# Kernel optimization log

Hardware: AMD Instinct MI355X
Metric: run time of the kernel (lower is better)

The kernel has to match this reference:

```python
import jax, jax.numpy as jnp
import numpy as np

D = 256    # lstm_encoder_size
B = 1024   # batch (number of agents/trajectories)
T = 512    # prediction horizon (recurrence steps)
EPS = 1e-5


def setup_inputs() -> dict:
    key = jax.random.key(0)
    k = jax.random.split(key, 10)
    s = 1.0 / np.sqrt(D)
    return {
        "KS_ALL": jax.random.normal(k[0], (1, B, D), jnp.float32),
        "next_vf": jax.random.normal(k[1], (B, T), jnp.float32),
        # Koopman operators (torch Linear stores [out, in]; no bias)
        "A_w": jax.random.normal(k[2], (D, D), jnp.float32) * (0.4 * s),  # contractive
        "B_w": jax.random.normal(k[3], (D, 1), jnp.float32) * s,
        # decoder params (liner_dec=False)
        "W0": jax.random.normal(k[4], (2 * D, D), jnp.float32) * s,
        "b0": jnp.zeros((2 * D,), jnp.float32),
        "W1": jax.random.normal(k[5], (D, 2 * D), jnp.float32) / np.sqrt(2.0 * D),
        "b1": jnp.zeros((D,), jnp.float32),
        "ln_g": jnp.ones((D,), jnp.float32),
        "ln_b": jnp.zeros((D,), jnp.float32),
        "W2": jax.random.normal(k[6], (D, D), jnp.float32) * s,
        "b2": jnp.zeros((D,), jnp.float32),
        "W3": jax.random.normal(k[7], (3, D), jnp.float32) * s,
        "b3": jnp.zeros((3,), jnp.float32),
    }


def _layer_norm(x, g, b):
    mu = jnp.mean(x, axis=-1, keepdims=True)
    var = jnp.var(x, axis=-1, keepdims=True)
    return (x - mu) * jax.lax.rsqrt(var + EPS) * g + b


def reference(KS_ALL, next_vf, A_w, B_w, W0, b0, W1, b1, ln_g, ln_b, W2, b2, W3, b3):
    # train_flag=True -> use only the first time slice of KS_ALL
    ks0 = KS_ALL[0]                 # [B, D]
    u = next_vf.T                   # [T, B] time-major, matches permute(1,0,2)
    b_vec = B_w[:, 0]               # [D]  (Linear(1, D) on scalar input)

    def step(ks, u_t):
        ks_new = ks @ A_w.T + u_t[:, None] * b_vec[None, :]  # [B, D]
        return ks_new, ks_new

    _, ks_seq = jax.lax.scan(step, ks0, u)                   # [T, B, D]
    KS_pre = jnp.concatenate([ks0[None], ks_seq], axis=0)    # [T+1, B, D]

    # nonlinear decoder (eval mode: dropout is identity; use_elu=True)
    s1 = jnp.tanh(KS_pre @ W0.T + b0)          # [T+1, B, 2D]
    s2 = jnp.tanh(s1 @ W1.T + b1)              # [T+1, B, D]
    s2 = _layer_norm(KS_pre + s2, ln_g, ln_b)  # AddAndNorm
    s3 = jax.nn.elu(s2 @ W2.T + b2)
    OS = s3 @ W3.T + b3                        # [T+1, B, 3]
    return KS_pre, OS
```

## Files before the change

### kernel.cpp

```cpp
#include <hip/hip_runtime.h>

typedef unsigned short u16;
typedef __attribute__((ext_vector_type(8))) short bf16x8;
typedef __attribute__((ext_vector_type(4))) short bf16x4;
typedef __attribute__((ext_vector_type(4))) float f32x4;

#define MFMA16(a, b, c) __builtin_amdgcn_mfma_f32_16x16x32_bf16((a), (b), (c), 0, 0, 0)

#define OFF_UPAD 0
#define OFF_KS0  589824
#define OFF_W0   851968
#define OFF_W1   983040
#define OFF_W2   1114112
#define OFF_CRT  1179648
#define OFF_P    1196032
#define OS_OFF   134479872

__device__ __forceinline__ u16 f2bf(float f) {
  union { float f; unsigned int i; } v; v.f = f;
  return (u16)((v.i + 0x7fffu + ((v.i >> 16) & 1u)) >> 16);
}
__device__ __forceinline__ float bf2f(u16 u) {
  union { unsigned int i; float f; } v; v.i = ((unsigned int)u) << 16;
  return v.f;
}
__device__ __forceinline__ float fast_tanh(float x) {
  float e = __expf(2.0f * x);
  return 1.0f - __fdividef(2.0f, e + 1.0f);
}

__global__ void k_prep(const float* __restrict__ KS_ALL, const float* __restrict__ next_vf,
                       const float* __restrict__ A_w, const float* __restrict__ W0,
                       const float* __restrict__ W1, const float* __restrict__ W2,
                       u16* __restrict__ ws) {
  int idx = blockIdx.x * 256 + threadIdx.x;
  if (idx < 589824) {
    int r = idx / 576, c = idx % 576;
    ws[OFF_UPAD + idx] = (c < 64) ? (u16)0 : f2bf(next_vf[r * 512 + c - 64]);
    return;
  }
  idx -= 589824;
  if (idx < 262144) { ws[OFF_KS0 + idx] = f2bf(KS_ALL[idx]); return; }
  idx -= 262144;
  if (idx < 131072) { ws[OFF_W0 + idx] = f2bf(W0[idx]); return; }
  idx -= 131072;
  if (idx < 131072) { ws[OFF_W1 + idx] = f2bf(W1[idx]); return; }
  idx -= 131072;
  if (idx < 65536)  { ws[OFF_W2 + idx] = f2bf(W2[idx]); return; }
  idx -= 65536;
  if (idx < 65536) {
    int r = idx >> 8, c = idx & 255;
    ws[OFF_P + idx] = (r == c) ? (u16)0x3F80 : (u16)0;
    ws[OFF_P + 65536 + idx] = f2bf(A_w[idx]);
  }
}

__global__ __launch_bounds__(512) void k_pow(u16* __restrict__ ws, int s) {
  const u16* P = ws + OFF_P;
  int j = blockIdx.y + 1;
  int mh = blockIdx.x;
  int lane = threadIdx.x & 63, w = threadIdx.x >> 6;
  int wm = w >> 2, wn = w & 3;
  int lg = lane >> 4, ll = lane & 15;
  const u16* Am = P + s * 65536;
  const u16* Bm = P + j * 65536;
  f32x4 acc[4][4];
  f32x4 z = {0.f, 0.f, 0.f, 0.f};
#pragma unroll
  for (int mi = 0; mi < 4; ++mi)
#pragma unroll
    for (int ni = 0; ni < 4; ++ni) acc[mi][ni] = z;
#pragma unroll
  for (int ks = 0; ks < 8; ++ks) {
    bf16x8 a[4], b[4];
    int kk = ks * 32 + lg * 8;
#pragma unroll
    for (int mi = 0; mi < 4; ++mi) {
      int row = mh * 128 + wm * 64 + mi * 16 + ll;
      a[mi] = *(const bf16x8*)(Am + row * 256 + kk);
    }
#pragma unroll
    for (int ni = 0; ni < 4; ++ni) {
      int col = wn * 64 + ni * 16 + ll;
#pragma unroll
      for (int e = 0; e < 8; ++e) b[ni][e] = (short)Bm[(kk + e) * 256 + col];
    }
#pragma unroll
    for (int mi = 0; mi < 4; ++mi)
#pragma unroll
      for (int ni = 0; ni < 4; ++ni) acc[mi][ni] = MFMA16(a[mi], b[ni], acc[mi][ni]);
  }
  u16* Pd = ws + OFF_P + (s + j) * 65536;
#pragma unroll
  for (int mi = 0; mi < 4; ++mi)
#pragma unroll
    for (int ni = 0; ni < 4; ++ni)
#pragma unroll
      for (int r = 0; r < 4; ++r) {
        int row = mh * 128 + wm * 64 + mi * 16 + lg * 4 + r;
        int col = wn * 64 + ni * 16 + ll;
        Pd[row * 256 + col] = f2bf(acc[mi][ni][r]);
      }
}

__global__ void k_crevt(const float* __restrict__ B_w, u16* __restrict__ ws) {
  int s = blockIdx.x;
  int n = threadIdx.x;
  const u16* Pr = ws + OFF_P + (63 - s) * 65536 + n * 256;
  float acc = 0.f;
  for (int k = 0; k < 256; ++k) acc += bf2f(Pr[k]) * B_w[k];
  ws[OFF_CRT + n * 64 + s] = f2bf(acc);
}

__global__ __launch_bounds__(512) void k_fused(
    const u16* __restrict__ ws,
    const float* __restrict__ b0, const float* __restrict__ b1,
    const float* __restrict__ lng, const float* __restrict__ lnb,
    const float* __restrict__ b2, const float* __restrict__ W3,
    const float* __restrict__ b3, float* __restrict__ out) {
  __shared__ __align__(16) u16 Xb[16896];
  __shared__ __align__(16) unsigned char Hraw[33792];
  __shared__ float par[2308];
  u16* Hb = (u16*)Hraw;
  float* Hf = (float*)Hraw;

  float* pb0 = par;
  float* pb1 = par + 512;
  float* pg  = par + 768;
  float* pbt = par + 1024;
  float* pb2 = par + 1280;
  float* pW3 = par + 1536;
  float* pb3 = par + 2304;

  const int t  = blockIdx.y;
  const int R0 = blockIdx.x * 64;
  const int tid = threadIdx.x;
  const int lane = tid & 63, w = tid >> 6;
  const int lg = lane >> 4, ll = lane & 15;

  pb0[tid] = b0[tid];
  if (tid < 256) { pb1[tid] = b1[tid]; pg[tid] = lng[tid]; pbt[tid] = lnb[tid]; pb2[tid] = b2[tid]; }
  if (tid < 512) pW3[tid] = W3[tid];
  if (tid < 256) pW3[512 + tid] = W3[512 + tid];
  if (tid < 4) pb3[tid] = (tid < 3) ? b3[tid] : 0.f;

  f32x4 z = {0.f, 0.f, 0.f, 0.f};

  f32x4 acc[4][2];
#pragma unroll
  for (int mi = 0; mi < 4; ++mi)
#pragma unroll
    for (int ni = 0; ni < 2; ++ni) acc[mi][ni] = z;
  {
    const u16* CrevT = ws + OFF_CRT;
    bf16x8 au[4][2];
#pragma unroll
    for (int mi = 0; mi < 4; ++mi)
#pragma unroll
      for (int ksu = 0; ksu < 2; ++ksu) {
        const u16* up = ws + OFF_UPAD + (R0 + mi * 16 + ll) * 576 + t + ksu * 32 + lg * 8;
#pragma unroll
        for (int e = 0; e < 8; ++e) au[mi][ksu][e] = (short)up[e];
      }
#pragma unroll
    for (int ksu = 0; ksu < 2; ++ksu)
#pragma unroll
      for (int ni = 0; ni < 2; ++ni) {
        int n = w * 32 + ni * 16 + ll;
        bf16x8 bfr = *(const bf16x8*)(CrevT + n * 64 + ksu * 32 + lg * 8);
#pragma unroll
        for (int mi = 0; mi < 4; ++mi) acc[mi][ni] = MFMA16(au[mi][ksu], bfr, acc[mi][ni]);
      }
    if (t < 64) {
      const u16* Pt = ws + OFF_P + t * 65536;
      const u16* ks0b = ws + OFF_KS0;
#pragma unroll
      for (int ks = 0; ks < 8; ++ks) {
        bf16x8 a[4], b[2];
#pragma unroll
        for (int mi = 0; mi < 4; ++mi)
          a[mi] = *(const bf16x8*)(ks0b + (R0 + mi * 16 + ll) * 256 + ks * 32 + lg * 8);
#pragma unroll
        for (int ni = 0; ni < 2; ++ni)
          b[ni] = *(const bf16x8*)(Pt + (w * 32 + ni * 16 + ll) * 256 + ks * 32 + lg * 8);
#pragma unroll
        for (int mi = 0; mi < 4; ++mi)
#pragma unroll
          for (int ni = 0; ni < 2; ++ni) acc[mi][ni] = MFMA16(a[mi], b[ni], acc[mi][ni]);
      }
    }
  }
  __syncthreads();

#pragma unroll 1
  for (int p = 0; p < 2; ++p) {
#pragma unroll
    for (int mi2 = 0; mi2 < 2; ++mi2) {
      int mi = p * 2 + mi2;
#pragma unroll
      for (int ni = 0; ni < 2; ++ni)
#pragma unroll
        for (int r = 0; r < 4; ++r)
          Hf[(mi2 * 16 + lg * 4 + r) * 260 + w * 32 + ni * 16 + ll] = acc[mi][ni][r];
    }
    __syncthreads();
    float* ob = out + (size_t)t * 262144 + (size_t)(R0 + p * 32) * 256;
#pragma unroll
    for (int it = 0; it < 4; ++it) {
      int idx = it * 512 + tid;
      int row = idx >> 6, c4 = idx & 63;
      f32x4 v = *(const f32x4*)(Hf + row * 260 + c4 * 4);
      *(f32x4*)(ob + row * 256 + c4 * 4) = v;
      int rl = p * 32 + row;
      bf16x4 h;
#pragma unroll
      for (int e = 0; e < 4; ++e) h[e] = (short)f2bf(v[e]);
      int byt = (((rl << 9) + ((c4 >> 1) << 4)) ^ ((rl & 7) << 4)) + ((c4 & 1) << 3);
      *(bf16x4*)(Xb + (byt >> 1)) = h;
    }
    __syncthreads();
  }

  const u16* W0b = ws + OFF_W0;
  const u16* W1b = ws + OFF_W1;
  f32x4 accL2[4][2];
#pragma unroll
  for (int mi = 0; mi < 4; ++mi)
#pragma unroll
    for (int ni = 0; ni < 2; ++ni) accL2[mi][ni] = z;

#pragma unroll 1
  for (int h = 0; h < 2; ++h) {
#pragma unroll
    for (int mi = 0; mi < 4; ++mi)
#pragma unroll
      for (int ni = 0; ni < 2; ++ni) acc[mi][ni] = z;
#pragma unroll
    for (int ks = 0; ks < 8; ++ks) {
      bf16x8 a[4], b[2];
#pragma unroll
      for (int mi = 0; mi < 4; ++mi) {
        int rl = mi * 16 + ll;
        int byt = ((rl << 9) + ks * 64 + (lg << 4)) ^ ((rl & 7) << 4);
        a[mi] = *(const bf16x8*)(Xb + (byt >> 1));
      }
#pragma unroll
      for (int ni = 0; ni < 2; ++ni) {
        int n = h * 256 + w * 32 + ni * 16 + ll;
        b[ni] = *(const bf16x8*)(W0b + n * 256 + ks * 32 + lg * 8);
      }
#pragma unroll
      for (int mi = 0; mi < 4; ++mi)
#pragma unroll
        for (int ni = 0; ni < 2; ++ni) acc[mi][ni] = MFMA16(a[mi], b[ni], acc[mi][ni]);
    }
#pragma unroll
    for (int mi = 0; mi < 4; ++mi)
#pragma unroll
      for (int ni = 0; ni < 2; ++ni)
#pragma unroll
        for (int r = 0; r < 4; ++r) {
          int rl = mi * 16 + lg * 4 + r;
          int col_l = w * 32 + ni * 16 + ll;
          float v = fast_tanh(acc[mi][ni][r] + pb0[h * 256 + col_l]);
          int byt = ((rl << 9) + (col_l << 1)) ^ ((rl & 7) << 4);
          Hb[byt >> 1] = f2bf(v);
        }
    __syncthreads();
#pragma unroll
    for (int ks = 0; ks < 8; ++ks) {
      bf16x8 a[4], b[2];
#pragma unroll
      for (int mi = 0; mi < 4; ++mi) {
        int rl = mi * 16 + ll;
        int byt = ((rl << 9) + ks * 64 + (lg << 4)) ^ ((rl & 7) << 4);
        a[mi] = *(const bf16x8*)(Hb + (byt >> 1));
      }
#pragma unroll
      for (int ni = 0; ni < 2; ++ni) {
        int n = w * 32 + ni * 16 + ll;
        b[ni] = *(const bf16x8*)(W1b + n * 512 + h * 256 + ks * 32 + lg * 8);
      }
#pragma unroll
      for (int mi = 0; mi < 4; ++mi)
#pragma unroll
        for (int ni = 0; ni < 2; ++ni) accL2[mi][ni] = MFMA16(a[mi], b[ni], accL2[mi][ni]);
    }
    __syncthreads();
  }

#pragma unroll
  for (int mi = 0; mi < 4; ++mi)
#pragma unroll
    for (int ni = 0; ni < 2; ++ni)
#pragma unroll
      for (int r = 0; r < 4; ++r) {
        int rl = mi * 16 + lg * 4 + r;
        int col = w * 32 + ni * 16 + ll;
        float v = fast_tanh(accL2[mi][ni][r] + pb1[col]);
        int bx = ((rl << 9) + (col << 1)) ^ ((rl & 7) << 4);
        v += bf2f(Xb[bx >> 1]);
        Hb[rl * 264 + col] = f2bf(v);
      }
  __syncthreads();

  {
    int row = tid >> 3, jq = tid & 7;
    u16* hr = Hb + row * 264 + jq * 32;
    bf16x8 chv[4];
#pragma unroll
    for (int q = 0; q < 4; ++q) chv[q] = *(const bf16x8*)(hr + q * 8);
    float s = 0.f, ss = 0.f;
#pragma unroll
    for (int q = 0; q < 4; ++q)
#pragma unroll
      for (int e = 0; e < 8; ++e) { float v = bf2f((u16)chv[q][e]); s += v; ss += v * v; }
    s += __shfl_xor(s, 1);  s += __shfl_xor(s, 2);  s += __shfl_xor(s, 4);
    ss += __shfl_xor(ss, 1); ss += __shfl_xor(ss, 2); ss += __shfl_xor(ss, 4);
    float mu = s * 0.00390625f;
    float var = ss * 0.00390625f - mu * mu;
    float rstd = rsqrtf(var + 1e-5f);
#pragma unroll
    for (int q = 0; q < 4; ++q) {
      bf16x8 o;
#pragma unroll
      for (int e = 0; e < 8; ++e) {
        int col = jq * 32 + q * 8 + e;
        float v = (bf2f((u16)chv[q][e]) - mu) * rstd * pg[col] + pbt[col];
        o[e] = (short)f2bf(v);
      }
      *(bf16x8*)(hr + q * 8) = o;
    }
  }
  __syncthreads();

#pragma unroll
  for (int mi = 0; mi < 4; ++mi)
#pragma unroll
    for (int ni = 0; ni < 2; ++ni) acc[mi][ni] = z;
  {
    const u16* W2b = ws + OFF_W2;
#pragma unroll
    for (int ks = 0; ks < 8; ++ks) {
      bf16x8 a[4], b[2];
#pragma unroll
      for (int mi = 0; mi < 4; ++mi) {
        int rl = mi * 16 + ll;
        a[mi] = *(const bf16x8*)(Hb + rl * 264 + ks * 32 + lg * 8);
      }
#pragma unroll
      for (int ni = 0; ni < 2; ++ni) {
        int n = w * 32 + ni * 16 + ll;
        b[ni] = *(const bf16x8*)(W2b + n * 256 + ks * 32 + lg * 8);
      }
#pragma unroll
      for (int mi = 0; mi < 4; ++mi)
#pragma unroll
        for (int ni = 0; ni < 2; ++ni) acc[mi][ni] = MFMA16(a[mi], b[ni], acc[mi][ni]);
    }
  }
#pragma unroll
  for (int mi = 0; mi < 4; ++mi)
#pragma unroll
    for (int ni = 0; ni < 2; ++ni)
#pragma unroll
      for (int r = 0; r < 4; ++r) {
        int rl = mi * 16 + lg * 4 + r;
        int col = w * 32 + ni * 16 + ll;
        float v = acc[mi][ni][r] + pb2[col];
        v = v > 0.f ? v : (__expf(v) - 1.f);
        Xb[rl * 264 + col] = f2bf(v);
      }
  __syncthreads();

  {
    int row = tid >> 3, jq = tid & 7;
    const u16* xr = Xb + row * 264 + jq * 32;
    float d0 = 0.f, d1 = 0.f, d2 = 0.f;
#pragma unroll
    for (int q = 0; q < 4; ++q) {
      bf16x8 c = *(const bf16x8*)(xr + q * 8);
#pragma unroll
      for (int e = 0; e < 8; ++e) {
        float v = bf2f((u16)c[e]);
        int col = jq * 32 + q * 8 + e;
        d0 += v * pW3[col]; d1 += v * pW3[256 + col]; d2 += v * pW3[512 + col];
      }
    }
    d0 += __shfl_xor(d0, 1); d0 += __shfl_xor(d0, 2); d0 += __shfl_xor(d0, 4);
    d1 += __shfl_xor(d1, 1); d1 += __shfl_xor(d1, 2); d1 += __shfl_xor(d1, 4);
    d2 += __shfl_xor(d2, 1); d2 += __shfl_xor(d2, 2); d2 += __shfl_xor(d2, 4);
    if (jq == 0) {
      int grow = R0 + row;
      int ob = OS_OFF + t * 3072 + grow * 3;
      out[ob]     = d0 + pb3[0];
      out[ob + 1] = d1 + pb3[1];
      out[ob + 2] = d2 + pb3[2];
    }
  }
}

extern "C" void kernel_launch(void* const* d_in, const int* in_sizes, int n_in,
                              void* d_out, int out_size, void* d_ws, size_t ws_size,
                              hipStream_t stream) {
  const float* KS_ALL  = (const float*)d_in[0];
  const float* next_vf = (const float*)d_in[1];
  const float* A_w     = (const float*)d_in[2];
  const float* B_w     = (const float*)d_in[3];
  const float* W0      = (const float*)d_in[4];
  const float* b0      = (const float*)d_in[5];
  const float* W1      = (const float*)d_in[6];
  const float* b1      = (const float*)d_in[7];
  const float* lng     = (const float*)d_in[8];
  const float* lnb     = (const float*)d_in[9];
  const float* W2      = (const float*)d_in[10];
  const float* b2      = (const float*)d_in[11];
  const float* W3      = (const float*)d_in[12];
  const float* b3      = (const float*)d_in[13];
  u16* ws = (u16*)d_ws;
  float* out = (float*)d_out;

  k_prep<<<4864, 256, 0, stream>>>(KS_ALL, next_vf, A_w, W0, W1, W2, ws);
  for (int s = 1; s <= 32; s <<= 1)
    k_pow<<<dim3(2, s), 512, 0, stream>>>(ws, s);
  k_crevt<<<64, 256, 0, stream>>>(B_w, ws);
  k_fused<<<dim3(16, 513), 512, 0, stream>>>(ws, b0, b1, lng, lnb, b2, W3, b3, out);
}
```

Before: 1.626 ms.

## Split decoder first layer into four quarter chunks to cut register pressure

The W0/W1 stage now runs in four 128-column quarters instead of two 256-column halves. Each wave computes one 16-column slice per quarter into a smaller accumulator and writes a narrower hidden tile to shared memory. The prefix-scan operand loads and the W2 GEMM are reordered to keep fewer A and B fragments live at once, and one __syncthreads before the output-store loop is removed. The aim is to lower VGPR usage, which could raise occupancy or avoid spills, at the cost of more barriers and repeated W1 operand passes.

```diff
diff --git a/kernel.cpp b/kernel.cpp
--- a/kernel.cpp
+++ b/kernel.cpp
@@ -153,24 +153,23 @@
     for (int ni = 0; ni < 2; ++ni) acc[mi][ni] = z;
   {
     const u16* CrevT = ws + OFF_CRT;
-    bf16x8 au[4][2];
-#pragma unroll
-    for (int mi = 0; mi < 4; ++mi)
-#pragma unroll
-      for (int ksu = 0; ksu < 2; ++ksu) {
+#pragma unroll
+    for (int ksu = 0; ksu < 2; ++ksu) {
+      bf16x8 au[4];
+#pragma unroll
+      for (int mi = 0; mi < 4; ++mi) {
         const u16* up = ws + OFF_UPAD + (R0 + mi * 16 + ll) * 576 + t + ksu * 32 + lg * 8;
 #pragma unroll
-        for (int e = 0; e < 8; ++e) au[mi][ksu][e] = (short)up[e];
-      }
-#pragma unroll
-    for (int ksu = 0; ksu < 2; ++ksu)
+        for (int e = 0; e < 8; ++e) au[mi][e] = (short)up[e];
+      }
 #pragma unroll
       for (int ni = 0; ni < 2; ++ni) {
         int n = w * 32 + ni * 16 + ll;
         bf16x8 bfr = *(const bf16x8*)(CrevT + n * 64 + ksu * 32 + lg * 8);
 #pragma unroll
-        for (int mi = 0; mi < 4; ++mi) acc[mi][ni] = MFMA16(au[mi][ksu], bfr, acc[mi][ni]);
-      }
+        for (int mi = 0; mi < 4; ++mi) acc[mi][ni] = MFMA16(au[mi], bfr, acc[mi][ni]);
+      }
+    }
     if (t < 64) {
       const u16* Pt = ws + OFF_P + t * 65536;
       const u16* ks0b = ws + OFF_KS0;
@@ -190,7 +189,6 @@
       }
     }
   }
-  __syncthreads();
 
 #pragma unroll 1
   for (int p = 0; p < 2; ++p) {
@@ -229,62 +227,45 @@
 #pragma unroll
     for (int ni = 0; ni < 2; ++ni) accL2[mi][ni] = z;
 
+  const int colL1 = w * 16 + ll;
 #pragma unroll 1
-  for (int h = 0; h < 2; ++h) {
-#pragma unroll
-    for (int mi = 0; mi < 4; ++mi)
-#pragma unroll
-      for (int ni = 0; ni < 2; ++ni) acc[mi][ni] = z;
+  for (int q = 0; q < 4; ++q) {
+    f32x4 accQ[4];
+#pragma unroll
+    for (int mi = 0; mi < 4; ++mi) accQ[mi] = z;
 #pragma unroll
     for (int ks = 0; ks < 8; ++ks) {
-      bf16x8 a[4], b[2];
+      bf16x8 b = *(const bf16x8*)(W0b + (q * 128 + colL1) * 256 + ks * 32 + lg * 8);
 #pragma unroll
       for (int mi = 0; mi < 4; ++mi) {
         int rl = mi * 16 + ll;
         int byt = ((rl << 9) + ks * 64 + (lg << 4)) ^ ((rl & 7) << 4);
-        a[mi] = *(const bf16x8*)(Xb + (byt >> 1));
-      }
-#pragma unroll
-      for (int ni = 0; ni < 2; ++ni) {
-        int n = h * 256 + w * 32 + ni * 16 + ll;
-        b[ni] = *(const bf16x8*)(W0b + n * 256 + ks * 32 + lg * 8);
-      }
-#pragma unroll
-      for (int mi = 0; mi < 4; ++mi)
-#pragma unroll
-        for (int ni = 0; ni < 2; ++ni) acc[mi][ni] = MFMA16(a[mi], b[ni], acc[mi][ni]);
+        bf16x8 a = *(const bf16x8*)(Xb + (byt >> 1));
+        accQ[mi] = MFMA16(a, b, accQ[mi]);
+      }
     }
 #pragma unroll
     for (int mi = 0; mi < 4; ++mi)
 #pragma unroll
-      for (int ni = 0; ni < 2; ++ni)
-#pragma unroll
-        for (int r = 0; r < 4; ++r) {
-          int rl = mi * 16 + lg * 4 + r;
-          int col_l = w * 32 + ni * 16 + ll;
-          float v = fast_tanh(acc[mi][ni][r] + pb0[h * 256 + col_l]);
-          int byt = ((rl << 9) + (col_l << 1)) ^ ((rl & 7) << 4);
-          Hb[byt >> 1] = f2bf(v);
-        }
+      for (int r = 0; r < 4; ++r) {
+        int rl2 = mi * 16 + lg * 4 + r;
+        float v = fast_tanh(accQ[mi][r] + pb0[q * 128 + colL1]);
+        int byt = ((rl2 << 8) + (colL1 << 1)) ^ ((rl2 & 7) << 4);
+        Hb[byt >> 1] = f2bf(v);
+      }
     __syncthreads();
 #pragma unroll
-    for (int ks = 0; ks < 8; ++ks) {
-      bf16x8 a[4], b[2];
+    for (int ks2 = 0; ks2 < 4; ++ks2) {
+      bf16x8 bf0 = *(const bf16x8*)(W1b + (w * 32 + ll) * 512 + q * 128 + ks2 * 32 + lg * 8);
+      bf16x8 bf1 = *(const bf16x8*)(W1b + (w * 32 + 16 + ll) * 512 + q * 128 + ks2 * 32 + lg * 8);
 #pragma unroll
       for (int mi = 0; mi < 4; ++mi) {
         int rl = mi * 16 + ll;
-        int byt = ((rl << 9) + ks * 64 + (lg << 4)) ^ ((rl & 7) << 4);
-        a[mi] = *(const bf16x8*)(Hb + (byt >> 1));
-      }
-#pragma unroll
-      for (int ni = 0; ni < 2; ++ni) {
-        int n = w * 32 + ni * 16 + ll;
-        b[ni] = *(const bf16x8*)(W1b + n * 512 + h * 256 + ks * 32 + lg * 8);
-      }
-#pragma unroll
-      for (int mi = 0; mi < 4; ++mi)
-#pragma unroll
-        for (int ni = 0; ni < 2; ++ni) accL2[mi][ni] = MFMA16(a[mi], b[ni], accL2[mi][ni]);
+        int byt = ((rl << 8) + ks2 * 64 + (lg << 4)) ^ ((rl & 7) << 4);
+        bf16x8 a = *(const bf16x8*)(Hb + (byt >> 1));
+        accL2[mi][0] = MFMA16(a, bf0, accL2[mi][0]);
+        accL2[mi][1] = MFMA16(a, bf1, accL2[mi][1]);
+      }
     }
     __syncthreads();
   }
@@ -334,43 +315,38 @@
   }
   __syncthreads();
 
-#pragma unroll
-  for (int mi = 0; mi < 4; ++mi)
-#pragma unroll
-    for (int ni = 0; ni < 2; ++ni) acc[mi][ni] = z;
   {
     const u16* W2b = ws + OFF_W2;
+    f32x4 a3[4][2];
+#pragma unroll
+    for (int mi = 0; mi < 4; ++mi)
+#pragma unroll
+      for (int ni = 0; ni < 2; ++ni) a3[mi][ni] = z;
 #pragma unroll
     for (int ks = 0; ks < 8; ++ks) {
-      bf16x8 a[4], b[2];
+      bf16x8 bf0 = *(const bf16x8*)(W2b + (w * 32 + ll) * 256 + ks * 32 + lg * 8);
+      bf16x8 bf1 = *(const bf16x8*)(W2b + (w * 32 + 16 + ll) * 256 + ks * 32 + lg * 8);
 #pragma unroll
       for (int mi = 0; mi < 4; ++mi) {
         int rl = mi * 16 + ll;
-        a[mi] = *(const bf16x8*)(Hb + rl * 264 + ks * 32 + lg * 8);
-      }
-#pragma unroll
-      for (int ni = 0; ni < 2; ++ni) {
-        int n = w * 32 + ni * 16 + ll;
-        b[ni] = *(const bf16x8*)(W2b + n * 256 + ks * 32 + lg * 8);
-      }
-#pragma unroll
-      for (int mi = 0; mi < 4; ++mi)
-#pragma unroll
-        for (int ni = 0; ni < 2; ++ni) acc[mi][ni] = MFMA16(a[mi], b[ni], acc[mi][ni]);
-    }
-  }
-#pragma unroll
-  for (int mi = 0; mi < 4; ++mi)
-#pragma unroll
-    for (int ni = 0; ni < 2; ++ni)
-#pragma unroll
-      for (int r = 0; r < 4; ++r) {
-        int rl = mi * 16 + lg * 4 + r;
-        int col = w * 32 + ni * 16 + ll;
-        float v = acc[mi][ni][r] + pb2[col];
-        v = v > 0.f ? v : (__expf(v) - 1.f);
-        Xb[rl * 264 + col] = f2bf(v);
-      }
+        bf16x8 a = *(const bf16x8*)(Hb + rl * 264 + ks * 32 + lg * 8);
+        a3[mi][0] = MFMA16(a, bf0, a3[mi][0]);
+        a3[mi][1] = MFMA16(a, bf1, a3[mi][1]);
+      }
+    }
+#pragma unroll
+    for (int mi = 0; mi < 4; ++mi)
+#pragma unroll
+      for (int ni = 0; ni < 2; ++ni)
+#pragma unroll
+        for (int r = 0; r < 4; ++r) {
+          int rl = mi * 16 + lg * 4 + r;
+          int col = w * 32 + ni * 16 + ll;
+          float v = a3[mi][ni][r] + pb2[col];
+          v = v > 0.f ? v : (__expf(v) - 1.f);
+          Xb[rl * 264 + col] = f2bf(v);
+        }
+  }
   __syncthreads();
 
   {
```

Result: no change. 1.604 ms (-1.4%).
